# Optimization experiments

Measured on AMD Instinct MI355X. Metric: run time of the kernel, lower is better.

## Reference

```python
import jax, jax.numpy as jnp
import numpy as np
import math

L = 6          # num_layers
D = 512        # hidden_dim
S = 2048       # seq_len
B = 8          # batch
ODIM = 1       # output_dim
SCALES = (24.0, 720.0)


def setup_inputs() -> dict:
    key = jax.random.key(0)
    ks = jax.random.split(key, 12)
    def n(k, shape, scale=0.02):
        return jax.random.normal(k, shape, dtype=jnp.float32) * scale
    return {
        "z": jax.random.normal(ks[0], (B, S, 1), dtype=jnp.float32),
        "c": jax.random.normal(ks[1], (B, S, 1), dtype=jnp.float32),
        "enc_w": n(ks[2], (D, 2)), "enc_b": jnp.zeros((D,), jnp.float32),
        "beta": jnp.ones((L, len(SCALES)), jnp.float32),
        "wq": n(ks[3], (L, D, D)), "bq": jnp.zeros((L, D), jnp.float32),
        "wk": n(ks[4], (L, D, D)), "bk": jnp.zeros((L, D), jnp.float32),
        "wv": n(ks[5], (L, D, D)), "bv": jnp.zeros((L, D), jnp.float32),
        "ln1_w": jnp.ones((L, D), jnp.float32), "ln1_b": jnp.zeros((L, D), jnp.float32),
        "ln2_w": jnp.ones((L, D), jnp.float32), "ln2_b": jnp.zeros((L, D), jnp.float32),
        "ff1_w": n(ks[6], (L, 4 * D, D)), "ff1_b": jnp.zeros((L, 4 * D), jnp.float32),
        "ff2_w": n(ks[7], (L, D, 4 * D)), "ff2_b": jnp.zeros((L, D), jnp.float32),
        "out_w": n(ks[8], (ODIM, D)), "out_b": jnp.zeros((ODIM,), jnp.float32),
    }


def _ln(x, w, b, eps=1e-5):
    m = jnp.mean(x, axis=-1, keepdims=True)
    v = jnp.var(x, axis=-1, keepdims=True)
    return (x - m) * jax.lax.rsqrt(v + eps) * w + b


def _posenc(seq_len, dim):
    pos = jnp.arange(seq_len, dtype=jnp.float32)[:, None]
    div = jnp.exp(jnp.arange(0, dim, 2, dtype=jnp.float32) * (-(math.log(10000.0) / dim)))
    pe = jnp.zeros((seq_len, dim), jnp.float32)
    pe = pe.at[:, 0::2].set(jnp.sin(pos * div))
    pe = pe.at[:, 1::2].set(jnp.cos(pos * div))
    return pe


def reference(z, c, enc_w, enc_b, beta, wq, bq, wk, bk, wv, bv,
              ln1_w, ln1_b, ln2_w, ln2_b, ff1_w, ff1_b, ff2_w, ff2_b,
              out_w, out_b):
    # SequenceEncoder: cat(z,c) -> Linear(2, D) -> + sinusoidal PE
    x = jnp.concatenate([z, c], axis=-1) @ enc_w.T + enc_b       # [B,S,D]
    seq_len, d = x.shape[1], x.shape[2]
    x = x + _posenc(seq_len, d)[None]
    sqrt_d = math.sqrt(d)

    idx = jnp.arange(seq_len, dtype=jnp.float32)
    dist = jnp.abs(idx[:, None] - idx[None, :])                  # [S,S]

    for l in range(L):
        # pre-norm with ln1 (applied twice in the original code - replicated)
        xn = _ln(x, ln1_w[l], ln1_b[l])
        Q = xn @ wq[l].T + bq[l]
        K = xn @ wk[l].T + bk[l]
        V = xn @ wv[l].T + bv[l]
        attn = jnp.einsum('bid,bjd->bij', Q, K) / sqrt_d          # [B,S,S]
        bias = beta[l, 0] * jnp.cos(2.0 * math.pi * dist / SCALES[0]) \
             + beta[l, 1] * jnp.cos(2.0 * math.pi * dist / SCALES[1])
        probs = jax.nn.softmax(attn + bias, axis=-1)
        att_out = jnp.einsum('bij,bjd->bid', probs, V)
        # original applies layer_norm_1 again to the residual sum
        x = _ln(x + att_out, ln1_w[l], ln1_b[l])
        xn2 = _ln(x, ln2_w[l], ln2_b[l])
        h = jax.nn.relu(xn2 @ ff1_w[l].T + ff1_b[l])
        x = x + h @ ff2_w[l].T + ff2_b[l]

    return x @ out_w.T + out_b                                    # [B,S,ODIM]
```

## Files before the change

kernel.cpp:

```cpp
#include <hip/hip_runtime.h>
#include <hip/hip_fp8.h>
#include <math.h>

#define BB 8
#define SS 2048
#define DD 512
#define LL 6
#define FFD 2048

typedef _Float16 half_t;
typedef __attribute__((ext_vector_type(8))) _Float16 half8;
typedef __attribute__((ext_vector_type(4))) float f32x4;

enum { EPI_NONE = 0, EPI_RELU = 2, EPI_RES = 3, EPI_ATTN = 4, EPI_QKV = 5, EPI_PV = 6 };

__device__ __forceinline__ unsigned char f2e4m3(float v) {
    __hip_fp8_e4m3 f(v);
    return f.__x;
}

__device__ __forceinline__ void gl_lds16(const void* g, void* l) {
    __builtin_amdgcn_global_load_lds(
        (const __attribute__((address_space(1))) unsigned int*)g,
        (__attribute__((address_space(3))) unsigned int*)l,
        16, 0, 0);
}

__device__ __forceinline__ void blockReduce2(float& a, float& b, float* sm) {
#pragma unroll
    for (int off = 32; off; off >>= 1) {
        a += __shfl_down(a, off);
        b += __shfl_down(b, off);
    }
    int lane = threadIdx.x & 63;
    int w = threadIdx.x >> 6;
    if (lane == 0) { sm[w] = a; sm[4 + w] = b; }
    __syncthreads();
    a = sm[0] + sm[1] + sm[2] + sm[3];
    b = sm[4] + sm[5] + sm[6] + sm[7];
    __syncthreads();
}

__global__ __launch_bounds__(256) void encode_kernel(
    const float* __restrict__ z, const float* __restrict__ c,
    const float* __restrict__ enc_w, const float* __restrict__ enc_b,
    float* __restrict__ x)
{
    int idx = blockIdx.x * 256 + threadIdx.x;
    int d  = idx & (DD - 1);
    int bs = idx >> 9;
    int s  = bs & (SS - 1);
    float v = z[bs] * enc_w[2 * d] + c[bs] * enc_w[2 * d + 1] + enc_b[d];
    float div = expf(-(float)(d & ~1) * (9.210340371976184f / 512.0f));
    float ang = (float)s * div;
    v += (d & 1) ? cosf(ang) : sinf(ang);
    x[idx] = v;
}

__global__ __launch_bounds__(256) void convert_layer_kernel(
    const float* __restrict__ wq, const float* __restrict__ wk,
    const float* __restrict__ wv, const float* __restrict__ f1,
    const float* __restrict__ f2, half_t* __restrict__ wqkv,
    half_t* __restrict__ f1h, half_t* __restrict__ f2h)
{
    const int NQ = DD * DD;
    int i = blockIdx.x * 256 + threadIdx.x;
    if (i < 3 * NQ) {
        int which = i >> 18, j = i & (NQ - 1);
        const float* s = (which == 0) ? wq : (which == 1) ? wk : wv;
        wqkv[i] = (half_t)s[j];
    } else {
        int k = i - 3 * NQ;
        if (k < FFD * DD) f1h[k] = (half_t)f1[k];
        else              f2h[k - FFD * DD] = (half_t)f2[k - FFD * DD];
    }
}

__global__ __launch_bounds__(256) void bias_table_kernel(
    const float* __restrict__ beta, float* __restrict__ tbl)
{
    int i = blockIdx.x * 256 + threadIdx.x;
    int l = i >> 11, d = i & (SS - 1);
    tbl[i] = beta[2 * l] * cosf(0.2617993877991494f * d)
           + beta[2 * l + 1] * cosf(0.008726646259971648f * d);
}

__global__ __launch_bounds__(256) void ln_kernel(
    const float* __restrict__ src, const float* __restrict__ w,
    const float* __restrict__ b, half_t* __restrict__ dst)
{
    __shared__ float sm[8];
    size_t row = blockIdx.x;
    const float* p = src + row * DD;
    int t = threadIdx.x;
    float v0 = p[t], v1 = p[t + 256];
    float s = v0 + v1, sq = v0 * v0 + v1 * v1;
    blockReduce2(s, sq, sm);
    float mean = s * (1.0f / DD);
    float var  = sq * (1.0f / DD) - mean * mean;
    float rs   = rsqrtf(var + 1e-5f);
    dst[row * DD + t]       = (half_t)((v0 - mean) * rs * w[t] + b[t]);
    dst[row * DD + t + 256] = (half_t)((v1 - mean) * rs * w[t + 256] + b[t + 256]);
}

__global__ __launch_bounds__(256) void ln_ln_kernel(
    float* __restrict__ x,
    const float* __restrict__ w1, const float* __restrict__ b1,
    const float* __restrict__ w2, const float* __restrict__ b2,
    half_t* __restrict__ xn)
{
    __shared__ float sm[8];
    size_t row = blockIdx.x;
    int t = threadIdx.x;
    float v0 = x[row * DD + t];
    float v1 = x[row * DD + t + 256];
    float s = v0 + v1, sq = v0 * v0 + v1 * v1;
    blockReduce2(s, sq, sm);
    float mean = s * (1.0f / DD);
    float var  = sq * (1.0f / DD) - mean * mean;
    float rs   = rsqrtf(var + 1e-5f);
    float y0 = (v0 - mean) * rs * w1[t] + b1[t];
    float y1 = (v1 - mean) * rs * w1[t + 256] + b1[t + 256];
    x[row * DD + t]       = y0;
    x[row * DD + t + 256] = y1;
    s = y0 + y1; sq = y0 * y0 + y1 * y1;
    blockReduce2(s, sq, sm);
    mean = s * (1.0f / DD);
    var  = sq * (1.0f / DD) - mean * mean;
    rs   = rsqrtf(var + 1e-5f);
    xn[row * DD + t]       = (half_t)((y0 - mean) * rs * w2[t] + b2[t]);
    xn[row * DD + t + 256] = (half_t)((y1 - mean) * rs * w2[t + 256] + b2[t + 256]);
}

template<typename TIN, int MT, int EPI, int SWZ = 0>
__global__ __launch_bounds__(256) void gemm_mfma(
    const void* __restrict__ Ap, const void* __restrict__ Wp,
    const float* __restrict__ bias, void* __restrict__ Cp,
    int N, int K, float alpha,
    long long sA, long long sW, long long sC,
    const float* __restrict__ biasK, const float* __restrict__ biasV,
    unsigned char* __restrict__ Ck, unsigned char* __restrict__ Cv)
{
    constexpr int TM = MT / 32;
    constexpr int ES = (int)sizeof(TIN);
    constexpr int BK = (ES == 2) ? 32 : 64;
    constexpr int NS = (ES == 2) ? 1 : 2;
    constexpr int ABYTES = MT * 64;
    constexpr int BBYTES = 128 * 64;
    __shared__ __align__(16) unsigned char As[2 * ABYTES];
    __shared__ __align__(16) unsigned char Bs[2 * BBYTES];

    int bxi, byi, bzi;
    if (SWZ == 1) {
        const int id = blockIdx.x;
        const int cc = id & 7, rr = id >> 3;
        bxi = rr & 15;
        const int ss = cc + 8 * (rr >> 4);
        byi = ss & 15; bzi = ss >> 4;
    } else { bxi = blockIdx.x; byi = blockIdx.y; bzi = blockIdx.z; }

    const int z = bzi;
    const unsigned char* A = (const unsigned char*)Ap + (size_t)z * sA * ES;
    const unsigned char* W = (const unsigned char*)Wp + (size_t)z * sW * ES;
    float*  Cf = (float*)Cp  + (size_t)z * sC;
    half_t* Ch = (half_t*)Cp + (size_t)z * sC;
    unsigned char* C8 = (unsigned char*)Cp + (size_t)z * sC;

    const int tid = threadIdx.x;
    const int wv = tid >> 6, ln = tid & 63;
    const int bm = bxi * MT, bn = byi * 128;
    const int wm = (wv & 1) * (MT / 2), wn = (wv >> 1) * 64;

    const int srow  = wv * 16 + (ln >> 2);
    const int scolB = (((ln & 3) ^ ((ln >> 3) & 3))) * 16;
    const unsigned char* Ag = A + (size_t)(bm + srow) * K * ES + scolB;
    const unsigned char* Bg = W + (size_t)(bn + srow) * K * ES + scolB;

    f32x4 acc[TM][4] = {};
    f32x4 accd[TM] = {};
    const long ONES8 = 0x3838383838383838L;

    const int lane15 = ln & 15, quad = ln >> 4;
    const int sw = (lane15 >> 1) & 3;
    const int nIter = K / BK;

    {
        unsigned char* la = As + wv * 1024;
        unsigned char* lb = Bs + wv * 1024;
        gl_lds16(Ag, la);
        if (MT == 128) gl_lds16(Ag + (size_t)64 * K * ES, la + 4096);
        gl_lds16(Bg, lb);
        gl_lds16(Bg + (size_t)64 * K * ES, lb + 4096);
    }
    __syncthreads();

    for (int it = 0; it < nIter; ++it) {
        const int cur = it & 1;
        if (it + 1 < nIter) {
            const size_t ko = (size_t)(it + 1) * 64;
            unsigned char* la = As + (cur ^ 1) * ABYTES + wv * 1024;
            unsigned char* lb = Bs + (cur ^ 1) * BBYTES + wv * 1024;
            gl_lds16(Ag + ko, la);
            if (MT == 128) gl_lds16(Ag + (size_t)64 * K * ES + ko, la + 4096);
            gl_lds16(Bg + ko, lb);
            gl_lds16(Bg + (size_t)64 * K * ES + ko, lb + 4096);
        }

        const unsigned char* Ab = As + cur * ABYTES;
        const unsigned char* Bb = Bs + cur * BBYTES;

        if constexpr (ES == 2) {
            const int cB = (quad ^ sw) * 16;
            half8 aF[TM], bF[4];
#pragma unroll
            for (int i = 0; i < TM; ++i)
                aF[i] = *(const half8*)(Ab + (wm + i * 16 + lane15) * 64 + cB);
#pragma unroll
            for (int j = 0; j < 4; ++j)
                bF[j] = *(const half8*)(Bb + (wn + j * 16 + lane15) * 64 + cB);
#pragma unroll
            for (int i = 0; i < TM; ++i)
#pragma unroll
                for (int j = 0; j < 4; ++j)
                    acc[i][j] = __builtin_amdgcn_mfma_f32_16x16x32_f16(
                        aF[i], bF[j], acc[i][j], 0, 0, 0);
        } else {
            long aF8[TM][NS], bF8[4][NS];
#pragma unroll
            for (int s = 0; s < NS; ++s) {
                const int cB = (((s * 2 + (quad >> 1)) ^ sw) * 16) + (quad & 1) * 8;
#pragma unroll
                for (int i = 0; i < TM; ++i)
                    aF8[i][s] = *(const long*)(Ab + (wm + i * 16 + lane15) * 64 + cB);
#pragma unroll
                for (int j = 0; j < 4; ++j)
                    bF8[j][s] = *(const long*)(Bb + (wn + j * 16 + lane15) * 64 + cB);
            }
#pragma unroll
            for (int s = 0; s < NS; ++s)
#pragma unroll
                for (int i = 0; i < TM; ++i) {
#pragma unroll
                    for (int j = 0; j < 4; ++j)
                        acc[i][j] = __builtin_amdgcn_mfma_f32_16x16x32_fp8_fp8(
                            aF8[i][s], bF8[j][s], acc[i][j], 0, 0, 0);
                    if (EPI == EPI_PV)
                        accd[i] = __builtin_amdgcn_mfma_f32_16x16x32_fp8_fp8(
                            aF8[i][s], ONES8, accd[i], 0, 0, 0);
                }
        }

        __syncthreads();
    }

    float invd[TM][4];
    if (EPI == EPI_PV) {
#pragma unroll
        for (int i = 0; i < TM; ++i)
#pragma unroll
            for (int r = 0; r < 4; ++r)
                invd[i][r] = 1.0f / accd[i][r];
    }

#pragma unroll
    for (int i = 0; i < TM; ++i) {
        const int m0 = bm + wm + i * 16 + quad * 4;
#pragma unroll
        for (int j = 0; j < 4; ++j) {
            const int gn = bn + wn + j * 16 + lane15;
            if (EPI == EPI_QKV) {
                const int seg = gn >> 9, nn = gn & (DD - 1);
                if (seg == 2) {
                    unsigned int pk = 0;
#pragma unroll
                    for (int r = 0; r < 4; ++r)
                        pk |= (unsigned int)f2e4m3(acc[i][j][r] + biasV[nn]) << (8 * r);
                    const int b = m0 >> 11, s0 = m0 & (SS - 1);
                    *(unsigned int*)&Cv[((size_t)b * DD + nn) * SS + s0] = pk;
                } else {
                    const float bs = (seg == 0) ? bias[nn] : biasK[nn];
                    unsigned char* dst = (seg == 0) ? C8 : Ck;
#pragma unroll
                    for (int r = 0; r < 4; ++r)
                        dst[(size_t)(m0 + r) * DD + nn] = f2e4m3(acc[i][j][r] + bs);
                }
            } else {
#pragma unroll
                for (int r = 0; r < 4; ++r) {
                    const int gm = m0 + r;
                    float v = acc[i][j][r];
                    if (EPI == EPI_ATTN) {
                        int dist = gm - gn; if (dist < 0) dist = -dist;
                        v = __expf(fminf(v * alpha + bias[dist], 6.0f));
                        C8[(size_t)gm * N + gn] = f2e4m3(v);
                    } else if (EPI == EPI_PV) {
                        const size_t idx = (size_t)gm * N + gn;
                        Cf[idx] = v * invd[i][r] + Cf[idx];
                    } else if (EPI == EPI_RELU) {
                        Ch[(size_t)gm * N + gn] = (half_t)fmaxf(v + bias[gn], 0.0f);
                    } else {
                        const size_t idx = (size_t)gm * N + gn;
                        Cf[idx] = v + bias[gn] + Cf[idx];
                    }
                }
            }
        }
    }
}

__global__ __launch_bounds__(256) void out_kernel(
    const float* __restrict__ x, const float* __restrict__ ow,
    const float* __restrict__ ob, float* __restrict__ out)
{
    int row = blockIdx.x * 4 + (threadIdx.x >> 6);
    int lane = threadIdx.x & 63;
    const float* p = x + (size_t)row * DD;
    float s = 0.f;
#pragma unroll
    for (int k = 0; k < 8; ++k) s += p[lane + 64 * k] * ow[lane + 64 * k];
#pragma unroll
    for (int off = 32; off; off >>= 1) s += __shfl_down(s, off);
    if (lane == 0) out[row] = s + ob[0];
}

extern "C" void kernel_launch(void* const* d_in, const int* in_sizes, int n_in,
                              void* d_out, int out_size, void* d_ws, size_t ws_size,
                              hipStream_t stream)
{
    (void)in_sizes; (void)n_in; (void)out_size; (void)ws_size;
    const float* z     = (const float*)d_in[0];
    const float* c     = (const float*)d_in[1];
    const float* enc_w = (const float*)d_in[2];
    const float* enc_b = (const float*)d_in[3];
    const float* beta  = (const float*)d_in[4];
    const float* wq    = (const float*)d_in[5];
    const float* bq    = (const float*)d_in[6];
    const float* wk    = (const float*)d_in[7];
    const float* bk    = (const float*)d_in[8];
    const float* wv    = (const float*)d_in[9];
    const float* bv    = (const float*)d_in[10];
    const float* ln1w  = (const float*)d_in[11];
    const float* ln1b  = (const float*)d_in[12];
    const float* ln2w  = (const float*)d_in[13];
    const float* ln2b  = (const float*)d_in[14];
    const float* ff1w  = (const float*)d_in[15];
    const float* ff1b  = (const float*)d_in[16];
    const float* ff2w  = (const float*)d_in[17];
    const float* ff2b  = (const float*)d_in[18];
    const float* ow    = (const float*)d_in[19];
    const float* ob    = (const float*)d_in[20];

    const size_t BSD = (size_t)BB * SS * DD;
    const size_t BSS = (size_t)BB * SS * SS;

    char* p = (char*)d_ws;
    float*  x    = (float*)p;  p += BSD * 4;
    half_t* xnh  = (half_t*)p; p += BSD * 2;
    unsigned char* sch = (unsigned char*)p; p += BSS;
    unsigned char* qh  = (unsigned char*)p; p += BSD;
    unsigned char* kh  = (unsigned char*)p; p += BSD;
    unsigned char* vth = (unsigned char*)p; p += BSD;
    half_t* hh   = (half_t*)p; p += (size_t)BB * SS * FFD * 2;
    half_t* wqkv = (half_t*)p; p += (size_t)3 * DD * DD * 2;
    half_t* f1h  = (half_t*)p; p += (size_t)FFD * DD * 2;
    half_t* f2h  = (half_t*)p; p += (size_t)FFD * DD * 2;
    float*  tbl  = (float*)p;

    const float alpha = 0.044194173824159216f;
    const int BS = BB * SS;
    const long long sQ = (long long)SS * DD, sP = (long long)SS * SS,
                    sV = (long long)DD * SS;
    const int CONV_BLKS = (3 * DD * DD + 2 * FFD * DD) / 256;

    bias_table_kernel<<<LL * SS / 256, 256, 0, stream>>>(beta, tbl);
    encode_kernel<<<BS * DD / 256, 256, 0, stream>>>(z, c, enc_w, enc_b, x);

    for (int l = 0; l < LL; ++l) {
        convert_layer_kernel<<<CONV_BLKS, 256, 0, stream>>>(
            wq + (size_t)l * DD * DD, wk + (size_t)l * DD * DD,
            wv + (size_t)l * DD * DD, ff1w + (size_t)l * FFD * DD,
            ff2w + (size_t)l * DD * FFD, wqkv, f1h, f2h);

        ln_kernel<<<BS, 256, 0, stream>>>(x, ln1w + l * DD, ln1b + l * DD, xnh);

        gemm_mfma<half_t, 128, EPI_QKV><<<dim3(BS / 128, 12, 1), 256, 0, stream>>>(
            xnh, wqkv, bq + l * DD, qh, 1536, DD, 0, 0, 0, 0,
            bk + l * DD, bv + l * DD, kh, vth);

        gemm_mfma<unsigned char, 128, EPI_ATTN, 1><<<dim3(2048, 1, 1), 256, 0, stream>>>(
            qh, kh, tbl + l * SS, sch, SS, DD, alpha, sQ, sQ, sP,
            nullptr, nullptr, nullptr, nullptr);

        gemm_mfma<unsigned char, 64, EPI_PV><<<dim3(SS / 64, DD / 128, BB), 256, 0, stream>>>(
            sch, vth, nullptr, x, DD, SS, 0, sP, sV, sQ,
            nullptr, nullptr, nullptr, nullptr);

        ln_ln_kernel<<<BS, 256, 0, stream>>>(x, ln1w + l * DD, ln1b + l * DD,
                                             ln2w + l * DD, ln2b + l * DD, xnh);

        gemm_mfma<half_t, 128, EPI_RELU><<<dim3(BS / 128, FFD / 128, 1), 256, 0, stream>>>(
            xnh, f1h, ff1b + l * FFD, hh, FFD, DD, 0, 0, 0, 0,
            nullptr, nullptr, nullptr, nullptr);
        gemm_mfma<half_t, 64, EPI_RES><<<dim3(BS / 64, DD / 128, 1), 256, 0, stream>>>(
            hh, f2h, ff2b + l * DD, x, DD, FFD, 0, 0, 0, 0,
            nullptr, nullptr, nullptr, nullptr);
    }

    out_kernel<<<BS / 4, 256, 0, stream>>>(x, ow, ob, (float*)d_out);
}
```

Measured before the change: 1.829 ms.

## Split-K the FF2 GEMM with atomic residual add and hoist FF weight conversion

The FF2 GEMM (K=2048) is now split into two K halves on a z-grid dimension, with each half atomically adding its partial into the residual x and only the first half adding the bias. A separate row stride (Kst) is added to the GEMM so that a split can index a sub-range of K. The FF1/FF2 weight conversion to fp16 is hoisted out of the layer loop into a single kernel that converts all layers up front, leaving only the QKV conversion per layer. This aims to raise occupancy for the small-N FF2 grid and cut per-layer conversion launches, at the cost of float atomics and nondeterministic summation order.

```diff
diff --git a/kernel.cpp b/kernel.cpp
--- a/kernel.cpp
+++ b/kernel.cpp
@@ -57,23 +57,25 @@
     x[idx] = v;
 }
 
-__global__ __launch_bounds__(256) void convert_layer_kernel(
+__global__ __launch_bounds__(256) void convert_ff_all_kernel(
+    const float* __restrict__ f1, const float* __restrict__ f2,
+    half_t* __restrict__ f1h, half_t* __restrict__ f2h)
+{
+    const size_t NF = (size_t)LL * FFD * DD;
+    size_t i = (size_t)blockIdx.x * 256 + threadIdx.x;
+    if (i < NF) f1h[i] = (half_t)f1[i];
+    else        f2h[i - NF] = (half_t)f2[i - NF];
+}
+
+__global__ __launch_bounds__(256) void convert_qkv_kernel(
     const float* __restrict__ wq, const float* __restrict__ wk,
-    const float* __restrict__ wv, const float* __restrict__ f1,
-    const float* __restrict__ f2, half_t* __restrict__ wqkv,
-    half_t* __restrict__ f1h, half_t* __restrict__ f2h)
+    const float* __restrict__ wv, half_t* __restrict__ wqkv)
 {
     const int NQ = DD * DD;
     int i = blockIdx.x * 256 + threadIdx.x;
-    if (i < 3 * NQ) {
-        int which = i >> 18, j = i & (NQ - 1);
-        const float* s = (which == 0) ? wq : (which == 1) ? wk : wv;
-        wqkv[i] = (half_t)s[j];
-    } else {
-        int k = i - 3 * NQ;
-        if (k < FFD * DD) f1h[k] = (half_t)f1[k];
-        else              f2h[k - FFD * DD] = (half_t)f2[k - FFD * DD];
-    }
+    int which = i >> 18, j = i & (NQ - 1);
+    const float* s = (which == 0) ? wq : (which == 1) ? wk : wv;
+    wqkv[i] = (half_t)s[j];
 }
 
 __global__ __launch_bounds__(256) void bias_table_kernel(
@@ -136,15 +138,14 @@
 __global__ __launch_bounds__(256) void gemm_mfma(
     const void* __restrict__ Ap, const void* __restrict__ Wp,
     const float* __restrict__ bias, void* __restrict__ Cp,
-    int N, int K, float alpha,
+    int N, int K, int Kst, float alpha,
     long long sA, long long sW, long long sC,
     const float* __restrict__ biasK, const float* __restrict__ biasV,
     unsigned char* __restrict__ Ck, unsigned char* __restrict__ Cv)
 {
     constexpr int TM = MT / 32;
     constexpr int ES = (int)sizeof(TIN);
-    constexpr int BK = (ES == 2) ? 32 : 64;
-    constexpr int NS = (ES == 2) ? 1 : 2;
+    constexpr int NS = 64 / (32 * ES);
     constexpr int ABYTES = MT * 64;
     constexpr int BBYTES = 128 * 64;
     __shared__ __align__(16) unsigned char As[2 * ABYTES];
@@ -173,24 +174,24 @@
 
     const int srow  = wv * 16 + (ln >> 2);
     const int scolB = (((ln & 3) ^ ((ln >> 3) & 3))) * 16;
-    const unsigned char* Ag = A + (size_t)(bm + srow) * K * ES + scolB;
-    const unsigned char* Bg = W + (size_t)(bn + srow) * K * ES + scolB;
+    const unsigned char* Ag = A + (size_t)(bm + srow) * Kst * ES + scolB;
+    const unsigned char* Bg = W + (size_t)(bn + srow) * Kst * ES + scolB;
 
     f32x4 acc[TM][4] = {};
     f32x4 accd[TM] = {};
     const long ONES8 = 0x3838383838383838L;
 
     const int lane15 = ln & 15, quad = ln >> 4;
-    const int sw = (lane15 >> 1) & 3;
-    const int nIter = K / BK;
+    const int swr = (lane15 >> 1) & 3;
+    const int nIter = (K * ES) / 64;
 
     {
         unsigned char* la = As + wv * 1024;
         unsigned char* lb = Bs + wv * 1024;
         gl_lds16(Ag, la);
-        if (MT == 128) gl_lds16(Ag + (size_t)64 * K * ES, la + 4096);
+        if (MT == 128) gl_lds16(Ag + (size_t)64 * Kst * ES, la + 4096);
         gl_lds16(Bg, lb);
-        gl_lds16(Bg + (size_t)64 * K * ES, lb + 4096);
+        gl_lds16(Bg + (size_t)64 * Kst * ES, lb + 4096);
     }
     __syncthreads();
 
@@ -201,16 +202,16 @@
             unsigned char* la = As + (cur ^ 1) * ABYTES + wv * 1024;
             unsigned char* lb = Bs + (cur ^ 1) * BBYTES + wv * 1024;
             gl_lds16(Ag + ko, la);
-            if (MT == 128) gl_lds16(Ag + (size_t)64 * K * ES + ko, la + 4096);
+            if (MT == 128) gl_lds16(Ag + (size_t)64 * Kst * ES + ko, la + 4096);
             gl_lds16(Bg + ko, lb);
-            gl_lds16(Bg + (size_t)64 * K * ES + ko, lb + 4096);
+            gl_lds16(Bg + (size_t)64 * Kst * ES + ko, lb + 4096);
         }
 
         const unsigned char* Ab = As + cur * ABYTES;
         const unsigned char* Bb = Bs + cur * BBYTES;
 
         if constexpr (ES == 2) {
-            const int cB = (quad ^ sw) * 16;
+            const int cB = (quad ^ swr) * 16;
             half8 aF[TM], bF[4];
 #pragma unroll
             for (int i = 0; i < TM; ++i)
@@ -225,16 +226,16 @@
                     acc[i][j] = __builtin_amdgcn_mfma_f32_16x16x32_f16(
                         aF[i], bF[j], acc[i][j], 0, 0, 0);
         } else {
-            long aF8[TM][NS], bF8[4][NS];
+            long aF8[NS][TM], bF8[NS][4];
 #pragma unroll
             for (int s = 0; s < NS; ++s) {
-                const int cB = (((s * 2 + (quad >> 1)) ^ sw) * 16) + (quad & 1) * 8;
+                const int cB = (((s * 2 + (quad >> 1)) ^ swr) * 16) + (quad & 1) * 8;
 #pragma unroll
                 for (int i = 0; i < TM; ++i)
-                    aF8[i][s] = *(const long*)(Ab + (wm + i * 16 + lane15) * 64 + cB);
+                    aF8[s][i] = *(const long*)(Ab + (wm + i * 16 + lane15) * 64 + cB);
 #pragma unroll
                 for (int j = 0; j < 4; ++j)
-                    bF8[j][s] = *(const long*)(Bb + (wn + j * 16 + lane15) * 64 + cB);
+                    bF8[s][j] = *(const long*)(Bb + (wn + j * 16 + lane15) * 64 + cB);
             }
 #pragma unroll
             for (int s = 0; s < NS; ++s)
@@ -243,10 +244,10 @@
 #pragma unroll
                     for (int j = 0; j < 4; ++j)
                         acc[i][j] = __builtin_amdgcn_mfma_f32_16x16x32_fp8_fp8(
-                            aF8[i][s], bF8[j][s], acc[i][j], 0, 0, 0);
+                            aF8[s][i], bF8[s][j], acc[i][j], 0, 0, 0);
                     if (EPI == EPI_PV)
                         accd[i] = __builtin_amdgcn_mfma_f32_16x16x32_fp8_fp8(
-                            aF8[i][s], ONES8, accd[i], 0, 0, 0);
+                            aF8[s][i], ONES8, accd[i], 0, 0, 0);
                 }
         }
 
@@ -300,7 +301,7 @@
                         Ch[(size_t)gm * N + gn] = (half_t)fmaxf(v + bias[gn], 0.0f);
                     } else {
                         const size_t idx = (size_t)gm * N + gn;
-                        Cf[idx] = v + bias[gn] + Cf[idx];
+                        atomicAdd(&Cf[idx], v + (z == 0 ? bias[gn] : 0.0f));
                     }
                 }
             }
@@ -352,6 +353,7 @@
 
     const size_t BSD = (size_t)BB * SS * DD;
     const size_t BSS = (size_t)BB * SS * SS;
+    const size_t NF  = (size_t)LL * FFD * DD;
 
     char* p = (char*)d_ws;
     float*  x    = (float*)p;  p += BSD * 4;
@@ -362,47 +364,47 @@
     unsigned char* vth = (unsigned char*)p; p += BSD;
     half_t* hh   = (half_t*)p; p += (size_t)BB * SS * FFD * 2;
     half_t* wqkv = (half_t*)p; p += (size_t)3 * DD * DD * 2;
-    half_t* f1h  = (half_t*)p; p += (size_t)FFD * DD * 2;
-    half_t* f2h  = (half_t*)p; p += (size_t)FFD * DD * 2;
+    half_t* f1h  = (half_t*)p; p += NF * 2;
+    half_t* f2h  = (half_t*)p; p += NF * 2;
     float*  tbl  = (float*)p;
 
     const float alpha = 0.044194173824159216f;
     const int BS = BB * SS;
     const long long sQ = (long long)SS * DD, sP = (long long)SS * SS,
                     sV = (long long)DD * SS;
-    const int CONV_BLKS = (3 * DD * DD + 2 * FFD * DD) / 256;
 
     bias_table_kernel<<<LL * SS / 256, 256, 0, stream>>>(beta, tbl);
+    convert_ff_all_kernel<<<(int)(2 * NF / 256), 256, 0, stream>>>(ff1w, ff2w, f1h, f2h);
     encode_kernel<<<BS * DD / 256, 256, 0, stream>>>(z, c, enc_w, enc_b, x);
 
     for (int l = 0; l < LL; ++l) {
-        convert_layer_kernel<<<CONV_BLKS, 256, 0, stream>>>(
+        convert_qkv_kernel<<<3 * DD * DD / 256, 256, 0, stream>>>(
             wq + (size_t)l * DD * DD, wk + (size_t)l * DD * DD,
-            wv + (size_t)l * DD * DD, ff1w + (size_t)l * FFD * DD,
-            ff2w + (size_t)l * DD * FFD, wqkv, f1h, f2h);
+            wv + (size_t)l * DD * DD, wqkv);
 
         ln_kernel<<<BS, 256, 0, stream>>>(x, ln1w + l * DD, ln1b + l * DD, xnh);
 
         gemm_mfma<half_t, 128, EPI_QKV><<<dim3(BS / 128, 12, 1), 256, 0, stream>>>(
-            xnh, wqkv, bq + l * DD, qh, 1536, DD, 0, 0, 0, 0,
+            xnh, wqkv, bq + l * DD, qh, 1536, DD, DD, 0, 0, 0, 0,
             bk + l * DD, bv + l * DD, kh, vth);
 
         gemm_mfma<unsigned char, 128, EPI_ATTN, 1><<<dim3(2048, 1, 1), 256, 0, stream>>>(
-            qh, kh, tbl + l * SS, sch, SS, DD, alpha, sQ, sQ, sP,
+            qh, kh, tbl + l * SS, sch, SS, DD, DD, alpha, sQ, sQ, sP,
             nullptr, nullptr, nullptr, nullptr);
 
         gemm_mfma<unsigned char, 64, EPI_PV><<<dim3(SS / 64, DD / 128, BB), 256, 0, stream>>>(
-            sch, vth, nullptr, x, DD, SS, 0, sP, sV, sQ,
+            sch, vth, nullptr, x, DD, SS, SS, 0, sP, sV, sQ,
             nullptr, nullptr, nullptr, nullptr);
 
         ln_ln_kernel<<<BS, 256, 0, stream>>>(x, ln1w + l * DD, ln1b + l * DD,
                                              ln2w + l * DD, ln2b + l * DD, xnh);
 
         gemm_mfma<half_t, 128, EPI_RELU><<<dim3(BS / 128, FFD / 128, 1), 256, 0, stream>>>(
-            xnh, f1h, ff1b + l * FFD, hh, FFD, DD, 0, 0, 0, 0,
+            xnh, f1h + (size_t)l * FFD * DD, ff1b + l * FFD, hh, FFD, DD, DD, 0, 0, 0, 0,
             nullptr, nullptr, nullptr, nullptr);
-        gemm_mfma<half_t, 64, EPI_RES><<<dim3(BS / 64, DD / 128, 1), 256, 0, stream>>>(
-            hh, f2h, ff2b + l * DD, x, DD, FFD, 0, 0, 0, 0,
+        gemm_mfma<half_t, 64, EPI_RES><<<dim3(BS / 64, DD / 128, 2), 256, 0, stream>>>(
+            hh, f2h + (size_t)l * DD * FFD, ff2b + l * DD, x, DD, FFD / 2, FFD, 0,
+            FFD / 2, FFD / 2, 0,
             nullptr, nullptr, nullptr, nullptr);
     }
 
```

Result: slower. 2.006 ms (+9.6%).
